# Kernel optimization log

Hardware: AMD Instinct MI355X
Metric: run time of the kernel (lower is better)

The kernel has to match this reference:

```python
import jax, jax.numpy as jnp
import numpy as np

EMB = 768
HEADS = 12
HEAD_DIM = EMB // HEADS
FF = 4 * EMB
EPS = 1e-5


def setup_inputs() -> dict:
    key = jax.random.key(0)
    ks = jax.random.split(key, 12)
    s = 0.02
    return {
        "x": jax.random.normal(ks[0], (4, 2048, EMB), dtype=jnp.float32),
        "ln1_scale": jnp.ones((EMB,), jnp.float32),
        "ln1_shift": jnp.zeros((EMB,), jnp.float32),
        # weights stored [in, out] (transpose of torch Linear layout)
        "wq": jax.random.normal(ks[1], (EMB, EMB), jnp.float32) * s,
        "wk": jax.random.normal(ks[2], (EMB, EMB), jnp.float32) * s,
        "wv": jax.random.normal(ks[3], (EMB, EMB), jnp.float32) * s,
        "wo": jax.random.normal(ks[4], (EMB, EMB), jnp.float32) * s,
        "bo": jnp.zeros((EMB,), jnp.float32),
        "ln2_scale": jnp.ones((EMB,), jnp.float32),
        "ln2_shift": jnp.zeros((EMB,), jnp.float32),
        "w1": jax.random.normal(ks[5], (EMB, FF), jnp.float32) * s,
        "b1": jnp.zeros((FF,), jnp.float32),
        "w2": jax.random.normal(ks[6], (FF, EMB), jnp.float32) * s,
        "b2": jnp.zeros((EMB,), jnp.float32),
    }


def _layernorm(x, scale, shift):
    mean = jnp.mean(x, axis=-1, keepdims=True)
    var = jnp.mean(jnp.square(x - mean), axis=-1, keepdims=True)  # unbiased=False
    return scale * (x - mean) / jnp.sqrt(var + EPS) + shift


def _gelu_tanh(x):
    c = jnp.sqrt(jnp.float32(2.0 / np.pi))
    return 0.5 * x * (1.0 + jnp.tanh(c * (x + 0.044715 * x * x * x)))


def _attention(x, wq, wk, wv, wo, bo):
    b, s, _ = x.shape
    q = (x @ wq).reshape(b, s, HEADS, HEAD_DIM).transpose(0, 2, 1, 3)
    k = (x @ wk).reshape(b, s, HEADS, HEAD_DIM).transpose(0, 2, 1, 3)
    v = (x @ wv).reshape(b, s, HEADS, HEAD_DIM).transpose(0, 2, 1, 3)
    scores = jnp.einsum("bhqd,bhkd->bhqk", q, k)  # [B,H,S,S]
    causal = jnp.tril(jnp.ones((s, s), dtype=bool))
    scores = jnp.where(causal, scores, -jnp.inf)
    weights = jax.nn.softmax(scores / jnp.sqrt(jnp.float32(HEAD_DIM)), axis=-1)
    ctx = jnp.einsum("bhqk,bhkd->bhqd", weights, v)
    ctx = ctx.transpose(0, 2, 1, 3).reshape(b, s, EMB)
    return ctx @ wo + bo


def reference(x, ln1_scale, ln1_shift, wq, wk, wv, wo, bo,
              ln2_scale, ln2_shift, w1, b1, w2, b2):
    # dropout rate is 0.0 (inference) -> identity
    x = x + _attention(_layernorm(x, ln1_scale, ln1_shift), wq, wk, wv, wo, bo)
    h = _layernorm(x, ln2_scale, ln2_shift)
    h = _gelu_tanh(h @ w1 + b1) @ w2 + b2
    return x + h
```

## Files before the change

### kernel.cpp

```cpp
#include <hip/hip_runtime.h>
#include <stdint.h>

#define EMB 768
#define SEQ 2048
#define BATCH 4
#define NHEADS 12
#define HDIM 64
#define FFDIM 3072
#define NTOK (BATCH*SEQ)
#define LNEPS 1e-5f
#define QSCALE 0.1803368801111137f

typedef __attribute__((ext_vector_type(8))) short bf16x8;
typedef __attribute__((ext_vector_type(4))) float f32x4;

__device__ __forceinline__ uint16_t f2bf(float f){
  union { float f; uint32_t u; } v; v.f = f;
  uint32_t r = v.u + 0x7fffu + ((v.u >> 16) & 1u);
  return (uint16_t)(r >> 16);
}
__device__ __forceinline__ uint32_t pk_rhu(float lo, float hi){
  union { float f; uint32_t u; } a, b; a.f = lo; b.f = hi;
  return __builtin_amdgcn_perm(b.u + 0x8000u, a.u + 0x8000u, 0x07060302u);
}

typedef __attribute__((address_space(3))) uint32_t lds32_t;
typedef __attribute__((address_space(1))) const uint32_t glb32_t;
__device__ __forceinline__ void gload16(const void* g, void* l){
  __builtin_amdgcn_global_load_lds((glb32_t*)(uintptr_t)g,
                                   (lds32_t*)(uintptr_t)l, 16, 0, 0);
}

struct TPtrs { const float* src[6]; uint16_t* dst[6]; };
__global__ __launch_bounds__(256) void transpose_all(TPtrs tp){
  int idx = blockIdx.x;
  int which, bx, by, K, N;
  if (idx < 2304){ which = idx/576; int l = idx - which*576; bx = l%24; by = l/24; K = 768;  N = 768;  }
  else if (idx < 4608){ which = 4; int l = idx-2304; bx = l%96; by = l/96; K = 768;  N = 3072; }
  else { which = 5; int l = idx-4608; bx = l%24; by = l/24; K = 3072; N = 768;  }
  const float* w = tp.src[which];
  uint16_t* wt   = tp.dst[which];
  __shared__ uint16_t tile[32][33];
  int n0 = bx*32, k0 = by*32;
  #pragma unroll
  for (int i=0;i<4;i++){
    int k = threadIdx.y + i*8;
    tile[k][threadIdx.x] = f2bf(w[(size_t)(k0+k)*N + n0 + threadIdx.x]);
  }
  __syncthreads();
  #pragma unroll
  for (int i=0;i<4;i++){
    int n = threadIdx.y + i*8;
    wt[(size_t)(n0+n)*K + k0 + threadIdx.x] = tile[threadIdx.x][n];
  }
}

__global__ __launch_bounds__(256) void ln_kernel(const float* __restrict__ x,
    const float* __restrict__ sc, const float* __restrict__ sh,
    uint16_t* __restrict__ out)
{
  int row = blockIdx.x*4 + (threadIdx.x>>6);
  int ln = threadIdx.x & 63;
  const float4* xr = (const float4*)(x + (size_t)row*EMB);
  float4 v0 = xr[ln], v1 = xr[64+ln], v2 = xr[128+ln];
  float s  = v0.x+v0.y+v0.z+v0.w + v1.x+v1.y+v1.z+v1.w + v2.x+v2.y+v2.z+v2.w;
  float s2 = v0.x*v0.x+v0.y*v0.y+v0.z*v0.z+v0.w*v0.w
           + v1.x*v1.x+v1.y*v1.y+v1.z*v1.z+v1.w*v1.w
           + v2.x*v2.x+v2.y*v2.y+v2.z*v2.z+v2.w*v2.w;
  #pragma unroll
  for (int off=1;off<64;off<<=1){ s += __shfl_xor(s,off); s2 += __shfl_xor(s2,off); }
  float mean = s*(1.f/768.f);
  float var  = s2*(1.f/768.f) - mean*mean;
  float rstd = rsqrtf(var + LNEPS);
  uint16_t* orow = out + (size_t)row*EMB;
  float4 vv[3] = {v0,v1,v2};
  #pragma unroll
  for (int i=0;i<3;i++){
    int c = (i*64+ln)*4;
    ushort4 o4;
    o4.x = f2bf((vv[i].x-mean)*rstd*sc[c+0] + sh[c+0]);
    o4.y = f2bf((vv[i].y-mean)*rstd*sc[c+1] + sh[c+1]);
    o4.z = f2bf((vv[i].z-mean)*rstd*sc[c+2] + sh[c+2]);
    o4.w = f2bf((vv[i].w-mean)*rstd*sc[c+3] + sh[c+3]);
    *(ushort4*)(orow + c) = o4;
  }
}

template<int MODE, int TM>
__global__ __launch_bounds__(256, 4) void gemm_bt(const uint16_t* __restrict__ A,
    const uint16_t* __restrict__ Bt0,
    const float* __restrict__ bias,
    const float* __restrict__ resid,
    void* __restrict__ outp,
    uint16_t* __restrict__ vt_out,
    int N, int K, long bt_zstride, long out_zstride)
{
  constexpr int MI = TM/32;
  __shared__ __align__(16) uint16_t As[2][TM][32];
  __shared__ __align__(16) uint16_t Bs[2][128][32];
  const uint16_t* Bt = Bt0 + (size_t)blockIdx.z * bt_zstride;
  int tid = threadIdx.x;
  int wave = tid>>6, ln = tid&63, lane16 = ln&15, quad = ln>>4;
  int m0 = blockIdx.x*TM, n0 = blockIdx.y*128;
  int wm = (wave>>1)*(MI*16), wn = (wave&1)*64;
  f32x4 zf = {0.f,0.f,0.f,0.f};
  f32x4 acc[MI][4];
  #pragma unroll
  for (int i=0;i<MI;i++)
    #pragma unroll
    for (int j=0;j<4;j++) acc[i][j]=zf;
  int ar = tid>>2;
  int ac = (tid&3)*8;
  const uint16_t* Arow0 = A  + (size_t)(m0+ar)*K    + ac;
  const uint16_t* Arow1 = A  + (size_t)(m0+ar+64)*K + ac;
  const uint16_t* Brow0 = Bt + (size_t)(n0+ar)*K    + ac;
  const uint16_t* Brow1 = Bt + (size_t)(n0+ar+64)*K + ac;

  auto stage = [&](int buf, int k0){
    char* lA = (char*)&As[buf][0][0] + wave*1024;
    char* lB = (char*)&Bs[buf][0][0] + wave*1024;
    gload16(Arow0 + k0, lA);
    if (TM==128) gload16(Arow1 + k0, lA + 4096);
    gload16(Brow0 + k0, lB);
    gload16(Brow1 + k0, lB + 4096);
  };

  int niter = K>>5;
  stage(0, 0);
  for (int s=0; s<niter; s++){
    __syncthreads();
    if (s+1 < niter) stage((s+1)&1, (s+1)<<5);
    int buf = s&1;
    bf16x8 af[MI], bfr[4];
    #pragma unroll
    for (int mi=0;mi<MI;mi++) af[mi]  = *(const bf16x8*)&As[buf][wm+mi*16+lane16][quad*8];
    #pragma unroll
    for (int ni=0;ni<4;ni++)  bfr[ni] = *(const bf16x8*)&Bs[buf][wn+ni*16+lane16][quad*8];
    #pragma unroll
    for (int mi=0;mi<MI;mi++)
      #pragma unroll
      for (int ni=0;ni<4;ni++)
        acc[mi][ni] = __builtin_amdgcn_mfma_f32_16x16x32_bf16(af[mi], bfr[ni], acc[mi][ni], 0,0,0);
  }
  if (MODE==0 && blockIdx.z==2){
    #pragma unroll
    for (int mi=0;mi<MI;mi++){
      int mrow0 = m0 + wm + mi*16 + quad*4;
      int bb = mrow0 >> 11, s = mrow0 & 2047;
      #pragma unroll
      for (int ni=0;ni<4;ni++){
        int ncol = n0 + wn + ni*16 + lane16;
        int hh = ncol >> 6, dd = ncol & 63;
        ushort4 o4 = { f2bf(acc[mi][ni][0]), f2bf(acc[mi][ni][1]),
                       f2bf(acc[mi][ni][2]), f2bf(acc[mi][ni][3]) };
        *(ushort4*)(vt_out + ((size_t)((bb*NHEADS+hh)*HDIM + dd))*SEQ + s) = o4;
      }
    }
    return;
  }
  float oscale = (MODE==0 && blockIdx.z==0) ? QSCALE : 1.0f;
  #pragma unroll
  for (int mi=0;mi<MI;mi++){
    #pragma unroll
    for (int r=0;r<4;r++){
      int mrow = m0 + wm + mi*16 + quad*4 + r;
      #pragma unroll
      for (int ni=0;ni<4;ni++){
        int ncol = n0 + wn + ni*16 + lane16;
        float vv = acc[mi][ni][r];
        size_t idx = (size_t)mrow*N + ncol;
        if (MODE==0){
          ((uint16_t*)outp)[(size_t)blockIdx.z*out_zstride + idx] = f2bf(vv*oscale);
        } else if (MODE==1){
          ((float*)outp)[idx] = vv + bias[ncol] + resid[idx];
        } else if (MODE==2){
          float t = vv + bias[ncol];
          float u = 1.5957691216057308f*(t + 0.044715f*t*t*t);
          ((uint16_t*)outp)[idx] = f2bf(t / (1.f + __expf(-u)));
        } else {
          ((float*)outp)[idx] = vv + bias[ncol] + resid[idx];
        }
      }
    }
  }
}

__global__ __launch_bounds__(256, 5) void attn_kernel(const uint16_t* __restrict__ q,
    const uint16_t* __restrict__ k, const uint16_t* __restrict__ vt,
    uint16_t* __restrict__ ctx)
{
  __shared__ __align__(16) uint16_t Ks[2][8][64][8];
  __shared__ __align__(16) uint16_t Vs[2][8][64][8];
  const f32x4 zf = {0.f,0.f,0.f,0.f};
  int tid = threadIdx.x;
  int wave = tid>>6, ln = tid&63, l16 = ln&15, quad = ln>>4;
  int id  = blockIdx.x;
  int xcd = id & 7;
  int r_  = id >> 3;
  int t   = 31 - (r_ / 6);
  int g   = xcd*6 + (r_ % 6);
  int h   = g % NHEADS, b = g / NHEADS;
  size_t kgbase = ((size_t)(b*SEQ + ln))*EMB + h*HDIM;
  size_t vgbase = ((size_t)((b*NHEADS + h)*HDIM + ln))*SEQ;

  f32x4 o[4];
  float m_l, l_l;
  bf16x8 qf0, qf1;
  int q0w, myq;

  auto stage = [&](int buf, int kv0){
    #pragma unroll
    for (int i=0;i<2;i++){
      int c = wave + 4*i;
      gload16(k  + kgbase + (size_t)kv0*EMB + c*8, &Ks[buf][c][0][0]);
      gload16(vt + vgbase + kv0 + c*8,             &Vs[buf][c][0][0]);
    }
  };
  auto init_tile = [&](int tile){
    q0w = tile*64 + wave*16;
    myq = q0w + l16;
    const uint16_t* qrow = q + ((size_t)(b*SEQ + q0w + l16))*EMB + h*HDIM + quad*8;
    qf0 = *(const bf16x8*)(qrow);
    qf1 = *(const bf16x8*)(qrow + 32);
    o[0]=zf; o[1]=zf; o[2]=zf; o[3]=zf;
    m_l = -3.0e38f; l_l = 0.f;
  };
  auto writeout = [&](){
    float inv = 1.0f / l_l;
    uint16_t* crow = ctx + ((size_t)(b*SEQ + q0w + l16))*EMB + h*HDIM + quad*4;
    #pragma unroll
    for (int tt=0; tt<4; tt++){
      ushort4 w4 = { f2bf(o[tt][0]*inv), f2bf(o[tt][1]*inv),
                     f2bf(o[tt][2]*inv), f2bf(o[tt][3]*inv) };
      *(ushort4*)(crow + tt*16) = w4;
    }
  };
  auto compute = [&](int buf, int kv0, bool masked){
    bf16x8 kf[4][2], vf[2][4];
    #pragma unroll
    for (int f=0; f<4; f++){
      kf[f][0] = *(const bf16x8*)&Ks[buf][quad  ][f*16+l16][0];
      kf[f][1] = *(const bf16x8*)&Ks[buf][quad+4][f*16+l16][0];
    }
    #pragma unroll
    for (int tt=0; tt<4; tt++){
      vf[0][tt] = *(const bf16x8*)&Vs[buf][quad  ][tt*16+l16][0];
      vf[1][tt] = *(const bf16x8*)&Vs[buf][quad+4][tt*16+l16][0];
    }
    f32x4 st[4];
    #pragma unroll
    for (int f=0; f<4; f++){
      st[f] = __builtin_amdgcn_mfma_f32_16x16x32_bf16(kf[f][0], qf0, zf, 0,0,0);
      st[f] = __builtin_amdgcn_mfma_f32_16x16x32_bf16(kf[f][1], qf1, st[f], 0,0,0);
    }
    if (masked){
      #pragma unroll
      for (int f=0; f<4; f++){
        int kvf = kv0 + f*16 + quad*4;
        #pragma unroll
        for (int r=0; r<4; r++)
          if (kvf + r > myq) st[f][r] = -1e30f;
      }
    }
    float cmax = -1e30f;
    #pragma unroll
    for (int f=0; f<4; f++)
      #pragma unroll
      for (int r=0; r<4; r++) cmax = fmaxf(cmax, st[f][r]);
    cmax = fmaxf(cmax, __shfl_xor(cmax,16));
    cmax = fmaxf(cmax, __shfl_xor(cmax,32));
    float mn = fmaxf(m_l, cmax);
    float alpha = __builtin_amdgcn_exp2f(m_l - mn);
    float rs = 0.f;
    #pragma unroll
    for (int f=0; f<4; f++)
      #pragma unroll
      for (int r=0; r<4; r++){
        st[f][r] = __builtin_amdgcn_exp2f(st[f][r] - mn);
        rs += st[f][r];
      }
    rs += __shfl_xor(rs,16); rs += __shfl_xor(rs,32);
    l_l = l_l*alpha + rs; m_l = mn;
    #pragma unroll
    for (int tt=0; tt<4; tt++)
      #pragma unroll
      for (int r=0; r<4; r++) o[tt][r] *= alpha;
    uint32_t dw[4][2];
    #pragma unroll
    for (int f=0; f<4; f++){
      dw[f][0] = pk_rhu(st[f][0], st[f][1]);
      dw[f][1] = pk_rhu(st[f][2], st[f][3]);
    }
    union { uint32_t u[4]; bf16x8 v; } pb[2];
    #pragma unroll
    for (int g2=0; g2<2; g2++)
      #pragma unroll
      for (int j=0; j<4; j++){
        int src = 16*(2*(quad&1) + (j>>1)) + l16;
        uint32_t lo = (uint32_t)__shfl((int)dw[2*g2  ][j&1], src, 64);
        uint32_t hi = (uint32_t)__shfl((int)dw[2*g2+1][j&1], src, 64);
        pb[g2].u[j] = (quad>>1) ? hi : lo;
      }
    #pragma unroll
    for (int tt=0; tt<4; tt++){
      o[tt] = __builtin_amdgcn_mfma_f32_16x16x32_bf16(vf[0][tt], pb[0].v, o[tt], 0,0,0);
      o[tt] = __builtin_amdgcn_mfma_f32_16x16x32_bf16(vf[1][tt], pb[1].v, o[tt], 0,0,0);
    }
  };

  init_tile(t);
  stage(0, 0);
  for (int s=0; s<=t; s++){
    __syncthreads();
    if (s+1 <= t) stage((s+1)&1, (s+1)*64);
    compute(s&1, s*64, s == t);
  }
  writeout();
}

extern "C" void kernel_launch(void* const* d_in, const int* in_sizes, int n_in,
                              void* d_out, int out_size, void* d_ws, size_t ws_size,
                              hipStream_t stream) {
  const float* x     = (const float*)d_in[0];
  const float* ln1_s = (const float*)d_in[1];
  const float* ln1_b = (const float*)d_in[2];
  const float* wq    = (const float*)d_in[3];
  const float* wk    = (const float*)d_in[4];
  const float* wv    = (const float*)d_in[5];
  const float* wo    = (const float*)d_in[6];
  const float* bo    = (const float*)d_in[7];
  const float* ln2_s = (const float*)d_in[8];
  const float* ln2_b = (const float*)d_in[9];
  const float* w1    = (const float*)d_in[10];
  const float* b1    = (const float*)d_in[11];
  const float* w2    = (const float*)d_in[12];
  const float* b2    = (const float*)d_in[13];

  uint16_t* wqkv_t = (uint16_t*)d_ws;
  uint16_t* wo_t   = wqkv_t + 3*EMB*EMB;
  uint16_t* w1_t   = wo_t   + EMB*EMB;
  uint16_t* w2_t   = w1_t   + (size_t)FFDIM*EMB;
  uint16_t* xn     = w2_t   + (size_t)EMB*FFDIM;
  uint16_t* qkv    = xn     + (size_t)NTOK*EMB;
  uint16_t* ctx    = qkv    + (size_t)3*NTOK*EMB;
  uint16_t* hff    = qkv;
  float*    x1     = (float*)(ctx + (size_t)NTOK*EMB);
  uint16_t* vt     = (uint16_t*)(x1 + (size_t)NTOK*EMB);

  TPtrs tp;
  tp.src[0]=wq; tp.src[1]=wk; tp.src[2]=wv; tp.src[3]=wo; tp.src[4]=w1; tp.src[5]=w2;
  tp.dst[0]=wqkv_t; tp.dst[1]=wqkv_t+EMB*EMB; tp.dst[2]=wqkv_t+2*EMB*EMB;
  tp.dst[3]=wo_t; tp.dst[4]=w1_t; tp.dst[5]=w2_t;
  transpose_all<<<6912, dim3(32,8), 0, stream>>>(tp);

  ln_kernel<<<NTOK/4, 256, 0, stream>>>(x, ln1_s, ln1_b, xn);
  gemm_bt<0,128><<<dim3(NTOK/128, EMB/128, 3), 256, 0, stream>>>(
      xn, wqkv_t, nullptr, nullptr, qkv, vt, EMB, EMB,
      (long)EMB*EMB, (long)NTOK*EMB);
  attn_kernel<<<1536, 256, 0, stream>>>(
      qkv, qkv + (size_t)NTOK*EMB, vt, ctx);
  gemm_bt<1,64><<<dim3(NTOK/64, EMB/128, 1), 256, 0, stream>>>(
      ctx, wo_t, bo, x, x1, nullptr, EMB, EMB, 0, 0);
  ln_kernel<<<NTOK/4, 256, 0, stream>>>(x1, ln2_s, ln2_b, xn);
  gemm_bt<2,128><<<dim3(NTOK/128, FFDIM/128, 1), 256, 0, stream>>>(
      xn, w1_t, b1, nullptr, hff, nullptr, FFDIM, EMB, 0, 0);
  gemm_bt<3,64><<<dim3(NTOK/64, EMB/128, 1), 256, 0, stream>>>(
      hff, w2_t, b2, x1, d_out, nullptr, EMB, FFDIM, 0, 0);
}
```

Before: 371.7 us.

## Add dedicated triple-buffered FFN1 GEMM kernel with async LDS loads

```diff
diff --git a/kernel.cpp b/kernel.cpp
--- a/kernel.cpp
+++ b/kernel.cpp
@@ -29,6 +29,12 @@
 __device__ __forceinline__ void gload16(const void* g, void* l){
   __builtin_amdgcn_global_load_lds((glb32_t*)(uintptr_t)g,
                                    (lds32_t*)(uintptr_t)l, 16, 0, 0);
+}
+
+__device__ __forceinline__ bf16x8 lds_read16(const void* p){
+  bf16x8 r; uint32_t off = (uint32_t)(uintptr_t)p;
+  asm volatile("ds_read_b128 %0, %1" : "=v"(r) : "v"(off));
+  return r;
 }
 
 struct TPtrs { const float* src[6]; uint16_t* dst[6]; };
@@ -185,6 +191,79 @@
   }
 }
 
+__global__ __launch_bounds__(256, 3) void gemm_ffn1(const uint16_t* __restrict__ A,
+    const uint16_t* __restrict__ Bt,
+    const float* __restrict__ bias,
+    uint16_t* __restrict__ outp)
+{
+  __shared__ __align__(16) uint16_t As[3][128][32];
+  __shared__ __align__(16) uint16_t Bs[3][128][32];
+  const int N = FFDIM, K = EMB;
+  int tid = threadIdx.x;
+  int wave = tid>>6, ln = tid&63, lane16 = ln&15, quad = ln>>4;
+  int m0 = blockIdx.x*128, n0 = blockIdx.y*128;
+  int wm = (wave>>1)*64, wn = (wave&1)*64;
+  f32x4 zf = {0.f,0.f,0.f,0.f};
+  f32x4 acc[4][4];
+  #pragma unroll
+  for (int i=0;i<4;i++)
+    #pragma unroll
+    for (int j=0;j<4;j++) acc[i][j]=zf;
+  int ar = tid>>2;
+  int ac = (tid&3)*8;
+  const uint16_t* Arow0 = A  + (size_t)(m0+ar)*K    + ac;
+  const uint16_t* Arow1 = A  + (size_t)(m0+ar+64)*K + ac;
+  const uint16_t* Brow0 = Bt + (size_t)(n0+ar)*K    + ac;
+  const uint16_t* Brow1 = Bt + (size_t)(n0+ar+64)*K + ac;
+
+  auto stage = [&](int buf, int k0){
+    char* lA = (char*)&As[buf][0][0] + wave*1024;
+    char* lB = (char*)&Bs[buf][0][0] + wave*1024;
+    gload16(Arow0 + k0, lA);
+    gload16(Arow1 + k0, lA + 4096);
+    gload16(Brow0 + k0, lB);
+    gload16(Brow1 + k0, lB + 4096);
+  };
+
+  const int niter = K>>5;
+  stage(0, 0);
+  stage(1, 32);
+  for (int s=0; s<niter; s++){
+    if (s+1 < niter) { asm volatile("s_waitcnt vmcnt(4)" ::: "memory"); }
+    else             { asm volatile("s_waitcnt vmcnt(0)" ::: "memory"); }
+    __builtin_amdgcn_s_barrier();
+    if (s+2 < niter) stage((s+2)%3, (s+2)<<5);
+    int buf = s%3;
+    __builtin_amdgcn_sched_barrier(0);
+    bf16x8 af[4], bfr[4];
+    #pragma unroll
+    for (int mi=0;mi<4;mi++) af[mi]  = lds_read16(&As[buf][wm+mi*16+lane16][quad*8]);
+    #pragma unroll
+    for (int ni=0;ni<4;ni++) bfr[ni] = lds_read16(&Bs[buf][wn+ni*16+lane16][quad*8]);
+    asm volatile("s_waitcnt lgkmcnt(0)" ::: "memory");
+    __builtin_amdgcn_sched_barrier(0);
+    #pragma unroll
+    for (int mi=0;mi<4;mi++)
+      #pragma unroll
+      for (int ni=0;ni<4;ni++)
+        acc[mi][ni] = __builtin_amdgcn_mfma_f32_16x16x32_bf16(af[mi], bfr[ni], acc[mi][ni], 0,0,0);
+  }
+  #pragma unroll
+  for (int mi=0;mi<4;mi++){
+    #pragma unroll
+    for (int r=0;r<4;r++){
+      int mrow = m0 + wm + mi*16 + quad*4 + r;
+      #pragma unroll
+      for (int ni=0;ni<4;ni++){
+        int ncol = n0 + wn + ni*16 + lane16;
+        float t = acc[mi][ni][r] + bias[ncol];
+        float u = 1.5957691216057308f*(t + 0.044715f*t*t*t);
+        outp[(size_t)mrow*N + ncol] = f2bf(t / (1.f + __expf(-u)));
+      }
+    }
+  }
+}
+
 __global__ __launch_bounds__(256, 5) void attn_kernel(const uint16_t* __restrict__ q,
     const uint16_t* __restrict__ k, const uint16_t* __restrict__ vt,
     uint16_t* __restrict__ ctx)
@@ -362,8 +441,7 @@
   gemm_bt<1,64><<<dim3(NTOK/64, EMB/128, 1), 256, 0, stream>>>(
       ctx, wo_t, bo, x, x1, nullptr, EMB, EMB, 0, 0);
   ln_kernel<<<NTOK/4, 256, 0, stream>>>(x1, ln2_s, ln2_b, xn);
-  gemm_bt<2,128><<<dim3(NTOK/128, FFDIM/128, 1), 256, 0, stream>>>(
-      xn, w1_t, b1, nullptr, hff, nullptr, FFDIM, EMB, 0, 0);
+  gemm_ffn1<<<dim3(NTOK/128, FFDIM/128), 256, 0, stream>>>(xn, w1_t, b1, hff);
   gemm_bt<3,64><<<dim3(NTOK/64, EMB/128, 1), 256, 0, stream>>>(
       hff, w2_t, b2, x1, d_out, nullptr, EMB, FFDIM, 0, 0);
 }
```

After: 373.5 us. No clear change (+0.5%).
